# Performance work log

Hardware: AMD Instinct MI355X
Metric: run time of the kernel (lower is better)

The kernel has to match this reference:

```python
import jax, jax.numpy as jnp
import numpy as np

B, N, D = 1, 4096, 1024
H, DK, DV = 8, 16, 64
DEPTH_FOR_INIT = 6
WINDOW_THRESHOLD = 256


def setup_inputs() -> dict:
    key = jax.random.key(0)
    ks = jax.random.split(key, 6)
    std = 0.1 / np.sqrt(D)  # init_normal_ uses last-dim (input dim) of weight
    q_w = jax.random.normal(ks[0], (D, H, DK)) * std
    g_w = jaxax_gw = jax.random.normal(ks[1], (D, H, DV)) * 0.1  # gate weights: plain std=0.1
    k_w = jax.random.normal(ks[2], (D, H, DK)) * std
    v_w = jax.random.normal(ks[3], (D, H, DV)) * std
    w_qg = jnp.concatenate([q_w, g_w], axis=-1)   # [D, H, DK+DV]
    w_kv = jnp.concatenate([k_w, v_w], axis=-1)   # [D, H, DK+DV]
    w_out = jax.random.normal(ks[4], (H * DV, D)) * (0.1 / np.sqrt(H * DV))
    tokens = jax.random.normal(ks[5], (B, N, D))
    log_window = jnp.linspace(0.0, float(np.log(WINDOW_THRESHOLD)), H)  # SoftMask.init_
    log_r = jnp.zeros(H)  # inverse_acceptance_width: log(1.0)
    log_hscale = jnp.full((H,), float(np.log(1.0 / np.sqrt(H * DEPTH_FOR_INIT))))
    return dict(tokens=tokens, w_qg=w_qg, w_kv=w_kv, w_out=w_out,
                log_window=log_window, log_r=log_r, log_hscale=log_hscale)


def _l2norm(t):
    n = jnp.linalg.norm(t, axis=-1, keepdims=True)
    return t / jnp.maximum(n, 1e-12)


def reference(tokens, w_qg, w_kv, w_out, log_window, log_r, log_hscale):
    # projections, split heads: [B, H, N, DK+DV]
    qg = jnp.einsum('bnd,dhk->bhnk', tokens, w_qg)
    kv = jnp.einsum('bnd,dhk->bhnk', tokens, w_kv)
    q, g = qg[..., :DK], qg[..., DK:]
    k, v = kv[..., :DK], kv[..., DK:]
    q, k, v = _l2norm(q), _l2norm(k), _l2norm(v)
    # cosine similarity [B, H, N, N]
    sim = jnp.einsum('bhid,bhjd->bhij', q, k)
    # relu^2 screening
    r = (jnp.exp(log_r) + 1.0)[None, :, None, None]
    attn = jnp.square(jax.nn.relu(1.0 - r * (1.0 - sim)))
    # learned distance-aware cosine soft mask (implies causality: distance<=0)
    pos = jnp.arange(N, dtype=jnp.float32)
    dist = pos[None, :] - pos[:, None]  # [i, j] -> j - i  (offset = 0, square attn)
    w = (jnp.exp(log_window) + 1.0)[:, None, None]  # [H,1,1]
    soft = jnp.where((dist[None] <= 0.0) & (dist[None] > -w),
                     0.5 * (jnp.cos(dist[None] * jnp.pi / w) + 1.0), 0.0)  # [H,N,N]
    attn = attn * soft[None]
    # aggregate values
    aggr = jnp.einsum('bhij,bhjd->bhid', attn, v)
    # tanh_norm
    norm = jnp.linalg.norm(aggr, axis=-1, keepdims=True)
    normed = jnp.tanh(norm) * (aggr / jnp.maximum(norm, 1e-12))
    # gating: tanh(silu(g)), then head-wise scale
    out = normed * jnp.tanh(jax.nn.silu(g))
    out = out * jnp.exp(log_hscale)[None, :, None, None]
    # merge heads: b h n d -> b n (h d)
    out = out.transpose(0, 2, 1, 3).reshape(B, N, H * DV)
    return out @ w_out
```

## Files before the change

kernel.cpp:

```cpp
#include <hip/hip_runtime.h>
#include <hip/hip_bf16.h>
#include <math.h>

#define N_TOK 4096
#define D_MODEL 1024
#define NHEAD 8
#define DKQ 16
#define DVH 64
#define QGW 80
#define QGN 640
#define HD  512
#define TI  32
#define DC  64
#define NCH_MAX 5
#define EPI_UNITS (3 * N_TOK / 4)

typedef __attribute__((ext_vector_type(8))) short short8;
typedef __attribute__((ext_vector_type(4))) float f32x4;

#define GLOAD_LDS16(gp, lp) \
  __builtin_amdgcn_global_load_lds((const __attribute__((address_space(1))) void*)(gp), \
                                   (__attribute__((address_space(3))) void*)(lp), 16, 0, 0)

__global__ __launch_bounds__(256) void pack_kernel(
    const float* __restrict__ tokens, const float* __restrict__ w_qg,
    const float* __restrict__ w_kv, const float* __restrict__ w_out,
    __hip_bfloat16* __restrict__ tokB, __hip_bfloat16* __restrict__ wqgT,
    __hip_bfloat16* __restrict__ wkvT, __hip_bfloat16* __restrict__ woutT)
{
    __shared__ float tile[32][33];
    int b = blockIdx.x;
    int t = threadIdx.x;

    if (b < 4096) {
        int i = (b * 256 + t) * 4;
        float4 v = *(const float4*)(tokens + i);
        __hip_bfloat16 o[4] = { __float2bfloat16(v.x), __float2bfloat16(v.y),
                                __float2bfloat16(v.z), __float2bfloat16(v.w) };
        *(ushort4*)(tokB + i) = *(const ushort4*)o;
        return;
    }

    const float* in; __hip_bfloat16* outp; int R, C, tb;
    b -= 4096;
    if (b < 640)       { in = w_qg;  outp = wqgT;  R = 1024; C = 640;  tb = b; }
    else if (b < 1280) { in = w_kv;  outp = wkvT;  R = 1024; C = 640;  tb = b - 640; }
    else               { in = w_out; outp = woutT; R = 512;  C = 1024; tb = b - 1280; }
    int ctiles = C / 32;
    int bx = (tb % ctiles) * 32;
    int by = (tb / ctiles) * 32;
    int tx = t & 31, ty = t >> 5;

    #pragma unroll
    for (int j = 0; j < 32; j += 8)
        tile[j + ty][tx] = in[(size_t)(by + j + ty) * C + bx + tx];
    __syncthreads();
    #pragma unroll
    for (int j = 0; j < 32; j += 8)
        outp[(size_t)(bx + j + ty) * R + by + tx] =
            __float2bfloat16(tile[tx][j + ty]);
}

__global__ __launch_bounds__(256) void gemm_mfma(
    const __hip_bfloat16* __restrict__ A,
    const __hip_bfloat16* __restrict__ Bt0, float* __restrict__ C0,
    const __hip_bfloat16* __restrict__ Bt1, float* __restrict__ C1,
    int Nb, int K, int ntiles_n)
{
    __shared__ __hip_bfloat16 As[2][128 * 32];
    __shared__ __hip_bfloat16 Bs[2][64 * 32];

    int t = threadIdx.x;
    int l = t & 63;
    int w = t >> 6;
    int wr = w >> 1, wc = w & 1;

    int bnt = blockIdx.x;
    const __hip_bfloat16* Bt = Bt0;
    float* C = C0;
    if (bnt >= ntiles_n) { Bt = Bt1; C = C1; bnt -= ntiles_n; }
    int bm = blockIdx.y * 128;
    int bn = bnt * 64;

    int srow = t >> 2;
    int skc  = (t & 3) * 8;
    const __hip_bfloat16* ga0 = A + (size_t)(bm + srow) * K + skc;
    const __hip_bfloat16* ga1 = A + (size_t)(bm + 64 + srow) * K + skc;
    const __hip_bfloat16* gb  = Bt + (size_t)(bn + srow) * K + skc;
    int ldst = (t & ~63) * 8;

    f32x4 acc[4][2] = {};

    int aro = (wr * 64 + (l & 15)) * 32 + (l >> 4) * 8;
    int bro = (wc * 32 + (l & 15)) * 32 + (l >> 4) * 8;

    for (int k0 = 0; k0 < K; k0 += 64) {
        GLOAD_LDS16(ga0 + k0,      &As[0][ldst]);
        GLOAD_LDS16(ga1 + k0,      &As[0][2048 + ldst]);
        GLOAD_LDS16(gb  + k0,      &Bs[0][ldst]);
        GLOAD_LDS16(ga0 + k0 + 32, &As[1][ldst]);
        GLOAD_LDS16(ga1 + k0 + 32, &As[1][2048 + ldst]);
        GLOAD_LDS16(gb  + k0 + 32, &Bs[1][ldst]);
        __syncthreads();

        #pragma unroll
        for (int kk = 0; kk < 2; ++kk) {
            short8 af[4], bf[2];
            #pragma unroll
            for (int m = 0; m < 4; ++m)
                af[m] = *(const short8*)&As[kk][aro + m * 16 * 32];
            #pragma unroll
            for (int n = 0; n < 2; ++n)
                bf[n] = *(const short8*)&Bs[kk][bro + n * 16 * 32];

            #pragma unroll
            for (int m = 0; m < 4; ++m)
                #pragma unroll
                for (int n = 0; n < 2; ++n)
                    acc[m][n] = __builtin_amdgcn_mfma_f32_16x16x32_bf16(
                                    af[m], bf[n], acc[m][n], 0, 0, 0);
        }
        __syncthreads();
    }

    int crow = bm + wr * 64 + (l >> 4) * 4;
    int ccol = bn + wc * 32 + (l & 15);
    #pragma unroll
    for (int m = 0; m < 4; ++m)
        #pragma unroll
        for (int n = 0; n < 2; ++n)
            #pragma unroll
            for (int j = 0; j < 4; ++j)
                C[(size_t)(crow + m * 16 + j) * Nb + ccol + n * 16] = acc[m][n][j];
}

__global__ __launch_bounds__(256) void attn_chunk_kernel(
    const float* __restrict__ qg, const float* __restrict__ kv,
    const float* __restrict__ log_window, const float* __restrict__ log_r,
    const float* __restrict__ log_hscale,
    float* __restrict__ Ypart, __hip_bfloat16* __restrict__ Yb)
{
    int bid = blockIdx.x;
    int h    = bid / (128 * NCH_MAX);
    int rem  = bid - h * (128 * NCH_MAX);
    int tile = rem / NCH_MAX;
    int slot = rem - tile * NCH_MAX;
    int i0 = tile * TI;
    int t = threadIdx.x;

    float w = expf(log_window[h]) + 1.f;
    float r = expf(log_r[h]) + 1.f;
    int dmax = (int)ceilf(w) - 1;
    int jstart = i0 - dmax; if (jstart < 0) jstart = 0;
    int nch = (i0 + TI - jstart + DC - 1) / DC;
    if (slot >= nch) return;
    int j0 = jstart + slot * DC;

    __shared__ float Q_lds[TI][16];
    __shared__ float K_lds[DC][16];
    __shared__ float V_lds[DC][DVH];
    __shared__ float att_lds[TI][68];
    __shared__ float soft_lds[288];

    const float PI = 3.14159265358979f;
    for (int d = t; d <= dmax; d += 256)
        soft_lds[d] = 0.5f * (cosf(PI * (float)d / w) + 1.f);

    if (t < TI * 4) {
        int iq = t >> 2, c = (t & 3) * 4;
        float4 qv = *(const float4*)(qg + (size_t)(i0 + iq) * QGN + h * QGW + c);
        float s = qv.x*qv.x + qv.y*qv.y + qv.z*qv.z + qv.w*qv.w;
        s += __shfl_xor(s, 1); s += __shfl_xor(s, 2);
        float inv = 1.f / fmaxf(sqrtf(s), 1e-12f);
        qv.x *= inv; qv.y *= inv; qv.z *= inv; qv.w *= inv;
        *(float4*)&Q_lds[iq][c] = qv;
    }
    {
        int jr = t >> 2, c = (t & 3) * 4;
        int j = j0 + jr;
        float4 kx = make_float4(0.f, 0.f, 0.f, 0.f);
        if (j < N_TOK)
            kx = *(const float4*)(kv + (size_t)j * QGN + h * QGW + c);
        float s = kx.x*kx.x + kx.y*kx.y + kx.z*kx.z + kx.w*kx.w;
        s += __shfl_xor(s, 1); s += __shfl_xor(s, 2);
        float inv = 1.f / fmaxf(sqrtf(s), 1e-12f);
        kx.x *= inv; kx.y *= inv; kx.z *= inv; kx.w *= inv;
        *(float4*)&K_lds[jr][c] = kx;
    }
    #pragma unroll
    for (int kk = 0; kk < 4; ++kk) {
        int f = t + kk * 256;
        int jc = f >> 4, c = (f & 15) * 4;
        int j = j0 + jc;
        float4 vx = make_float4(0.f, 0.f, 0.f, 0.f);
        if (j < N_TOK)
            vx = *(const float4*)(kv + (size_t)j * QGN + h * QGW + DKQ + c);
        float s = vx.x*vx.x + vx.y*vx.y + vx.z*vx.z + vx.w*vx.w;
        s += __shfl_xor(s, 1); s += __shfl_xor(s, 2);
        s += __shfl_xor(s, 4); s += __shfl_xor(s, 8);
        float inv = 1.f / fmaxf(sqrtf(s), 1e-12f);
        vx.x *= inv; vx.y *= inv; vx.z *= inv; vx.w *= inv;
        *(float4*)&V_lds[jc][c] = vx;
    }
    __syncthreads();

    int i_loc = t & 31;
    int jgrp  = t >> 5;
    int i_glob = i0 + i_loc;
    float q[16];
    #pragma unroll
    for (int c = 0; c < 16; ++c) q[c] = Q_lds[i_loc][c];

    #pragma unroll
    for (int jj = 0; jj < 8; ++jj) {
        int jc = jgrp * 8 + jj;
        int j = j0 + jc;
        int d = i_glob - j;
        float sim = 0.f;
        #pragma unroll
        for (int c4 = 0; c4 < 4; ++c4) {
            float4 kk4 = *(const float4*)&K_lds[jc][c4 * 4];
            sim += q[c4*4+0]*kk4.x + q[c4*4+1]*kk4.y
                 + q[c4*4+2]*kk4.z + q[c4*4+3]*kk4.w;
        }
        float a = fmaxf(1.f - r * (1.f - sim), 0.f);
        int dc = min(max(d, 0), dmax);
        bool valid = (d >= 0) && (d <= dmax);
        att_lds[i_loc][jc] = valid ? a * a * soft_lds[dc] : 0.f;
    }
    __syncthreads();

    int wv = t >> 6, ihalf = (t >> 5) & 1, dvp = t & 31;
    int ib = wv * 8 + ihalf * 4;
    float acc[4][2] = {};

    #pragma unroll
    for (int g4 = 0; g4 < 16; ++g4) {
        int jc0 = g4 * 4;
        float4 am[4];
        #pragma unroll
        for (int m = 0; m < 4; ++m)
            am[m] = *(const float4*)&att_lds[ib + m][jc0];
        float2 v0 = *(const float2*)&V_lds[jc0 + 0][dvp * 2];
        float2 v1 = *(const float2*)&V_lds[jc0 + 1][dvp * 2];
        float2 v2 = *(const float2*)&V_lds[jc0 + 2][dvp * 2];
        float2 v3 = *(const float2*)&V_lds[jc0 + 3][dvp * 2];
        #pragma unroll
        for (int m = 0; m < 4; ++m) {
            acc[m][0] += am[m].x * v0.x + am[m].y * v1.x
                       + am[m].z * v2.x + am[m].w * v3.x;
            acc[m][1] += am[m].x * v0.y + am[m].y * v1.y
                       + am[m].z * v2.y + am[m].w * v3.y;
        }
    }

    if (nch == 1) {
        float hs = expf(log_hscale[h]);
        #pragma unroll
        for (int m = 0; m < 4; ++m) {
            float ss = acc[m][0]*acc[m][0] + acc[m][1]*acc[m][1];
            #pragma unroll
            for (int off = 16; off; off >>= 1) ss += __shfl_xor(ss, off);
            float norm = sqrtf(ss);
            float scale = tanhf(norm) / fmaxf(norm, 1e-12f);
            int i = i0 + ib + m;
            float2 g2 = *(const float2*)(qg + (size_t)i * QGN + h * QGW + DKQ + dvp * 2);
            float gate0 = tanhf(g2.x / (1.f + expf(-g2.x)));
            float gate1 = tanhf(g2.y / (1.f + expf(-g2.y)));
            __hip_bfloat16 ob[2] = { __float2bfloat16(acc[m][0] * scale * gate0 * hs),
                                     __float2bfloat16(acc[m][1] * scale * gate1 * hs) };
            *(ushort2*)(Yb + (size_t)i * HD + h * DVH + dvp * 2) = *(const ushort2*)ob;
        }
    } else {
        #pragma unroll
        for (int m = 0; m < 4; ++m) {
            int i = i0 + ib + m;
            float2 st = make_float2(acc[m][0], acc[m][1]);
            *(float2*)(Ypart + ((size_t)slot * N_TOK + i) * HD + h * DVH + dvp * 2) = st;
        }
    }
}

__global__ __launch_bounds__(256) void attn_epilogue_kernel(
    const float* __restrict__ Ypart, const float* __restrict__ qg,
    const float* __restrict__ log_window, const float* __restrict__ log_hscale,
    __hip_bfloat16* __restrict__ Y)
{
    int wv = threadIdx.x >> 6, lane = threadIdx.x & 63;
    int gid = 5 * N_TOK + blockIdx.x * 4 + wv;
    int h = gid >> 12;
    int i = gid & (N_TOK - 1);

    float w  = expf(log_window[h]) + 1.f;
    int dmax = (int)ceilf(w) - 1;
    int i0 = i & ~(TI - 1);
    int jstart = i0 - dmax; if (jstart < 0) jstart = 0;
    int nch = (i0 + TI - jstart + DC - 1) / DC;
    if (nch < 2) return;

    float hs = expf(log_hscale[h]);
    size_t base = (size_t)i * HD + h * DVH + lane;
    float a = 0.f;
    for (int c = 0; c < nch; ++c)
        a += Ypart[(size_t)c * N_TOK * HD + base];

    float g = qg[(size_t)i * QGN + h * QGW + DKQ + lane];
    float gate = tanhf(g / (1.f + expf(-g)));

    float ss = a * a;
    #pragma unroll
    for (int off = 32; off; off >>= 1) ss += __shfl_xor(ss, off);
    float norm = sqrtf(ss);
    float scale = tanhf(norm) / fmaxf(norm, 1e-12f);

    float o = a * scale * gate * hs;
    Y[(size_t)i * HD + h * DVH + lane] = __float2bfloat16(o);
}

extern "C" void kernel_launch(void* const* d_in, const int* in_sizes, int n_in,
                              void* d_out, int out_size, void* d_ws, size_t ws_size,
                              hipStream_t stream)
{
    const float* tokens     = (const float*)d_in[0];
    const float* w_qg       = (const float*)d_in[1];
    const float* w_kv       = (const float*)d_in[2];
    const float* w_out      = (const float*)d_in[3];
    const float* log_window = (const float*)d_in[4];
    const float* log_r      = (const float*)d_in[5];
    const float* log_hscale = (const float*)d_in[6];
    float* out = (float*)d_out;

    char* ws = (char*)d_ws;
    float* qg = (float*)ws;            ws += (size_t)N_TOK * QGN * 4;
    float* kv = (float*)ws;            ws += (size_t)N_TOK * QGN * 4;
    __hip_bfloat16* tokB  = (__hip_bfloat16*)ws; ws += (size_t)N_TOK * D_MODEL * 2;
    __hip_bfloat16* wqgT  = (__hip_bfloat16*)ws; ws += (size_t)QGN * D_MODEL * 2;
    __hip_bfloat16* wkvT  = (__hip_bfloat16*)ws; ws += (size_t)QGN * D_MODEL * 2;
    __hip_bfloat16* woutT = (__hip_bfloat16*)ws; ws += (size_t)D_MODEL * HD * 2;
    __hip_bfloat16* Yb    = (__hip_bfloat16*)ws; ws += (size_t)N_TOK * HD * 2;
    float* Ypart = (float*)ws;         ws += (size_t)NCH_MAX * N_TOK * HD * 4;

    pack_kernel<<<5888, 256, 0, stream>>>(tokens, w_qg, w_kv, w_out,
                                          tokB, wqgT, wkvT, woutT);
    {
        dim3 grid(2 * (QGN / 64), N_TOK / 128);
        gemm_mfma<<<grid, 256, 0, stream>>>(tokB, wqgT, qg, wkvT, kv,
                                            QGN, D_MODEL, QGN / 64);
    }
    attn_chunk_kernel<<<NHEAD * (N_TOK / TI) * NCH_MAX, 256, 0, stream>>>(
        qg, kv, log_window, log_r, log_hscale, Ypart, Yb);
    attn_epilogue_kernel<<<EPI_UNITS, 256, 0, stream>>>(
        Ypart, qg, log_window, log_hscale, Yb);
    {
        dim3 grid(D_MODEL / 64, N_TOK / 128);
        gemm_mfma<<<grid, 256, 0, stream>>>(Yb, woutT, out, woutT, out,
                                            D_MODEL, HD, D_MODEL / 64);
    }
}
```

Measured before the change: 82.00 us.

## Double-buffer GEMM LDS staging and skip fully-masked key columns in attention chunks

The GEMM now double-buffers its LDS tiles, issuing the next K-slice's global-to-LDS loads before computing on the current one, so memory latency can overlap the MFMA work. The attention chunk kernel computes the last key column that can be causally valid for its query tile and skips loading, normalizing, scoring and aggregating columns beyond it. The LDS footprint of the GEMM doubles, which may lower occupancy. The attention aggregation loop loses full unrolling because its trip count is now dynamic.

Measured after the change: 80.68 us. Within noise of the previous version (-1.6%).

```diff
diff --git a/kernel.cpp b/kernel.cpp
--- a/kernel.cpp
+++ b/kernel.cpp
@@ -67,8 +67,8 @@
     const __hip_bfloat16* __restrict__ Bt1, float* __restrict__ C1,
     int Nb, int K, int ntiles_n)
 {
-    __shared__ __hip_bfloat16 As[2][128 * 32];
-    __shared__ __hip_bfloat16 Bs[2][64 * 32];
+    __shared__ __hip_bfloat16 As[2][2][128 * 32];
+    __shared__ __hip_bfloat16 Bs[2][2][64 * 32];
 
     int t = threadIdx.x;
     int l = t & 63;
@@ -89,29 +89,36 @@
     const __hip_bfloat16* gb  = Bt + (size_t)(bn + srow) * K + skc;
     int ldst = (t & ~63) * 8;
 
+#define STAGE(buf, k0) do { \
+    GLOAD_LDS16(ga0 + (k0),      &As[buf][0][ldst]); \
+    GLOAD_LDS16(ga1 + (k0),      &As[buf][0][2048 + ldst]); \
+    GLOAD_LDS16(gb  + (k0),      &Bs[buf][0][ldst]); \
+    GLOAD_LDS16(ga0 + (k0) + 32, &As[buf][1][ldst]); \
+    GLOAD_LDS16(ga1 + (k0) + 32, &As[buf][1][2048 + ldst]); \
+    GLOAD_LDS16(gb  + (k0) + 32, &Bs[buf][1][ldst]); } while (0)
+
     f32x4 acc[4][2] = {};
 
     int aro = (wr * 64 + (l & 15)) * 32 + (l >> 4) * 8;
     int bro = (wc * 32 + (l & 15)) * 32 + (l >> 4) * 8;
 
-    for (int k0 = 0; k0 < K; k0 += 64) {
-        GLOAD_LDS16(ga0 + k0,      &As[0][ldst]);
-        GLOAD_LDS16(ga1 + k0,      &As[0][2048 + ldst]);
-        GLOAD_LDS16(gb  + k0,      &Bs[0][ldst]);
-        GLOAD_LDS16(ga0 + k0 + 32, &As[1][ldst]);
-        GLOAD_LDS16(ga1 + k0 + 32, &As[1][2048 + ldst]);
-        GLOAD_LDS16(gb  + k0 + 32, &Bs[1][ldst]);
-        __syncthreads();
+    int nk = K >> 6;
+    STAGE(0, 0);
+    __syncthreads();
+
+    int cur = 0;
+    for (int it = 0; it < nk; ++it) {
+        if (it + 1 < nk) STAGE(cur ^ 1, (it + 1) << 6);
 
         #pragma unroll
         for (int kk = 0; kk < 2; ++kk) {
             short8 af[4], bf[2];
             #pragma unroll
             for (int m = 0; m < 4; ++m)
-                af[m] = *(const short8*)&As[kk][aro + m * 16 * 32];
+                af[m] = *(const short8*)&As[cur][kk][aro + m * 16 * 32];
             #pragma unroll
             for (int n = 0; n < 2; ++n)
-                bf[n] = *(const short8*)&Bs[kk][bro + n * 16 * 32];
+                bf[n] = *(const short8*)&Bs[cur][kk][bro + n * 16 * 32];
 
             #pragma unroll
             for (int m = 0; m < 4; ++m)
@@ -121,7 +128,9 @@
                                     af[m], bf[n], acc[m][n], 0, 0, 0);
         }
         __syncthreads();
-    }
+        cur ^= 1;
+    }
+#undef STAGE
 
     int crow = bm + wr * 64 + (l >> 4) * 4;
     int ccol = bn + wc * 32 + (l & 15);
@@ -155,6 +164,10 @@
     int nch = (i0 + TI - jstart + DC - 1) / DC;
     if (slot >= nch) return;
     int j0 = jstart + slot * DC;
+
+    int jc_hi  = min(DC, i0 + TI - j0);
+    int jc_pad = (jc_hi + 3) & ~3;
+    int g4_hi  = jc_pad >> 2;
 
     __shared__ float Q_lds[TI][16];
     __shared__ float K_lds[DC][16];
@@ -178,29 +191,33 @@
     {
         int jr = t >> 2, c = (t & 3) * 4;
         int j = j0 + jr;
-        float4 kx = make_float4(0.f, 0.f, 0.f, 0.f);
-        if (j < N_TOK)
-            kx = *(const float4*)(kv + (size_t)j * QGN + h * QGW + c);
-        float s = kx.x*kx.x + kx.y*kx.y + kx.z*kx.z + kx.w*kx.w;
-        s += __shfl_xor(s, 1); s += __shfl_xor(s, 2);
-        float inv = 1.f / fmaxf(sqrtf(s), 1e-12f);
-        kx.x *= inv; kx.y *= inv; kx.z *= inv; kx.w *= inv;
-        *(float4*)&K_lds[jr][c] = kx;
+        if (jr < jc_hi) {
+            float4 kx = make_float4(0.f, 0.f, 0.f, 0.f);
+            if (j < N_TOK)
+                kx = *(const float4*)(kv + (size_t)j * QGN + h * QGW + c);
+            float s = kx.x*kx.x + kx.y*kx.y + kx.z*kx.z + kx.w*kx.w;
+            s += __shfl_xor(s, 1); s += __shfl_xor(s, 2);
+            float inv = 1.f / fmaxf(sqrtf(s), 1e-12f);
+            kx.x *= inv; kx.y *= inv; kx.z *= inv; kx.w *= inv;
+            *(float4*)&K_lds[jr][c] = kx;
+        }
     }
     #pragma unroll
     for (int kk = 0; kk < 4; ++kk) {
         int f = t + kk * 256;
         int jc = f >> 4, c = (f & 15) * 4;
         int j = j0 + jc;
-        float4 vx = make_float4(0.f, 0.f, 0.f, 0.f);
-        if (j < N_TOK)
-            vx = *(const float4*)(kv + (size_t)j * QGN + h * QGW + DKQ + c);
-        float s = vx.x*vx.x + vx.y*vx.y + vx.z*vx.z + vx.w*vx.w;
-        s += __shfl_xor(s, 1); s += __shfl_xor(s, 2);
-        s += __shfl_xor(s, 4); s += __shfl_xor(s, 8);
-        float inv = 1.f / fmaxf(sqrtf(s), 1e-12f);
-        vx.x *= inv; vx.y *= inv; vx.z *= inv; vx.w *= inv;
-        *(float4*)&V_lds[jc][c] = vx;
+        if (jc < jc_pad) {
+            float4 vx = make_float4(0.f, 0.f, 0.f, 0.f);
+            if (j < N_TOK)
+                vx = *(const float4*)(kv + (size_t)j * QGN + h * QGW + DKQ + c);
+            float s = vx.x*vx.x + vx.y*vx.y + vx.z*vx.z + vx.w*vx.w;
+            s += __shfl_xor(s, 1); s += __shfl_xor(s, 2);
+            s += __shfl_xor(s, 4); s += __shfl_xor(s, 8);
+            float inv = 1.f / fmaxf(sqrtf(s), 1e-12f);
+            vx.x *= inv; vx.y *= inv; vx.z *= inv; vx.w *= inv;
+            *(float4*)&V_lds[jc][c] = vx;
+        }
     }
     __syncthreads();
 
@@ -214,6 +231,7 @@
     #pragma unroll
     for (int jj = 0; jj < 8; ++jj) {
         int jc = jgrp * 8 + jj;
+        if (jc >= jc_pad) break;
         int j = j0 + jc;
         int d = i_glob - j;
         float sim = 0.f;
@@ -234,8 +252,7 @@
     int ib = wv * 8 + ihalf * 4;
     float acc[4][2] = {};
 
-    #pragma unroll
-    for (int g4 = 0; g4 < 16; ++g4) {
+    for (int g4 = 0; g4 < g4_hi; ++g4) {
         int jc0 = g4 * 4;
         float4 am[4];
         #pragma unroll
```
